# Performance work log

Hardware: AMD Instinct MI355X
Metric: run time of the kernel (lower is better)

The kernel has to match this reference:

```python
import jax, jax.numpy as jnp
import numpy as np

H = 512  # hidden_size
A = 1.0  # hard_sigm slope


def hard_sigm(a, x):
    return jnp.clip((a * x + 1.0) / 2.0, 0.0, 1.0)


def setup_inputs() -> dict:
    key = jax.random.key(0)
    ks = jax.random.split(key, 10)
    B = 8192
    bottom, top = 512, 512
    stdv = 1.0 / np.sqrt(H)
    u = lambda k, shp: jax.random.uniform(k, shp, jnp.float32, -stdv, stdv)
    return {
        "c": jax.random.normal(ks[0], (H, B), jnp.float32),
        "h_bottom": jax.random.normal(ks[1], (bottom, B), jnp.float32),
        "h": jax.random.normal(ks[2], (H, B), jnp.float32),
        "h_top": jax.random.normal(ks[3], (top, B), jnp.float32),
        "z": jax.random.uniform(ks[4], (1, B), jnp.float32),
        "z_bottom": jax.random.uniform(ks[5], (1, B), jnp.float32),
        "U_11": u(ks[6], (4 * H + 1, H)),
        "U_21": u(ks[7], (4 * H + 1, top)),
        "W_01": u(ks[8], (4 * H + 1, bottom)),
        "bias": u(ks[9], (4 * H + 1,)),
    }


def reference(c, h_bottom, h, h_top, z, z_bottom, U_11, U_21, W_01, bias):
    # z, z_bottom: (1, B) boundary indicators broadcast over the gate axis
    s_recur = (1.0 - z) * (U_11 @ h)          # (4H+1, B)
    s_topdown = z * (U_21 @ h_top)            # last_layer=False
    s_bottomup = z_bottom * (W_01 @ h_bottom)
    f_s = s_recur + s_topdown + s_bottomup + bias[:, None]

    f = jax.nn.sigmoid(f_s[0:H, :])
    i = jax.nn.sigmoid(f_s[H:2 * H, :])
    o = jax.nn.sigmoid(f_s[2 * H:3 * H, :])
    g = jnp.tanh(f_s[3 * H:4 * H, :])
    z_hat = hard_sigm(A, f_s[4 * H:4 * H + 1, :])  # (1, B)

    ig = i * g
    c_new = z * ig + (1.0 - z) * (1.0 - z_bottom) * c \
        + (1.0 - z) * z_bottom * (f * c + ig)
    tanh_c = jnp.tanh(c_new)
    h_new = z * o * tanh_c + (1.0 - z) * (1.0 - z_bottom) * h \
        + (1.0 - z) * z_bottom * o * tanh_c
    return (h_new, c_new, z_hat)
```

## Files before the change

kernel.cpp:

```cpp
#include <hip/hip_runtime.h>
#include <hip/hip_bf16.h>

#define HH 512
#define BB 8192
#define KK 1536
#define NT 48
#define HB 4194304
#define BLOB 8192

typedef __bf16 bhalf;
typedef __bf16 bf16x8 __attribute__((ext_vector_type(8)));
typedef float  f32x4  __attribute__((ext_vector_type(4)));

typedef __attribute__((address_space(1))) void* as1_t;
typedef __attribute__((address_space(3))) void* as3_t;

#define GLDS(src, dst) __builtin_amdgcn_global_load_lds((as1_t)(void*)(src), (as3_t)(void*)(dst), 16, 0, 0)
#define SBAR() asm volatile("s_barrier" ::: "memory")
#define VM0()  asm volatile("s_waitcnt vmcnt(0)" ::: "memory")


__global__ __launch_bounds__(256) void prep_all(
    const float* __restrict__ h, const float* __restrict__ ht,
    const float* __restrict__ hb, const float* __restrict__ z,
    const float* __restrict__ zb, const float* __restrict__ U11,
    const float* __restrict__ U21, const float* __restrict__ W01,
    bhalf* __restrict__ XtP, bhalf* __restrict__ WcP,
    float* __restrict__ zpart)
{
    const int tid = threadIdx.x;
    const int b   = blockIdx.x;

    if (b < 1536) {
        __shared__ float tile[32][257];
        const int kt = b % 48;
        const int nt = b / 48;
        const int n  = nt * 256 + tid;
        const int kb = kt * 32;

        const float* src; const float* wsrc; int kr; float scale;
        if (kb < 512)       { src = h;  wsrc = U11 + (size_t)2048 * 512 + kb;
                              kr = kb;        scale = 1.f - z[n]; }
        else if (kb < 1024) { src = ht; wsrc = U21 + (size_t)2048 * 512 + (kb - 512);
                              kr = kb - 512;  scale = z[n]; }
        else                { src = hb; wsrc = W01 + (size_t)2048 * 512 + (kb - 1024);
                              kr = kb - 1024; scale = zb[n]; }

        float zp = 0.f;
        #pragma unroll
        for (int kk = 0; kk < 32; ++kk) {
            const float v = src[(size_t)(kr + kk) * BB + n] * scale;
            tile[kk][tid] = v;
            zp += v * wsrc[kk];
        }
        zpart[(size_t)kt * BB + n] = zp;
        __syncthreads();

        bhalf* blob = XtP + (size_t)(nt * NT + kt) * BLOB;
        #pragma unroll
        for (int q = 0; q < 4; ++q) {
            const int s  = q * 256 + tid;
            const int rb = s >> 6, w = s & 63;
            const int hh = w >> 4, lrr = w & 15;
            const int nloc = rb * 16 + lrr, kloc = hh * 8;
            bf16x8 r;
            #pragma unroll
            for (int e = 0; e < 8; ++e) r[e] = (bhalf)tile[kloc + e][nloc];
            *(bf16x8*)(blob + s * 8) = r;
        }
    } else {
        const int o    = (b - 1536) * 4 + (tid >> 6);
        const int lane = tid & 63;
        const int g = o >> 9, j = o & 511;
        const int mp = 4 * j + g;
        const int mt = mp >> 8, rb = (mp >> 4) & 15, lrr = mp & 15;

        #pragma unroll
        for (int p = 0; p < 3; ++p) {
            const float* src = (p == 0) ? U11 : (p == 1) ? U21 : W01;
            const float* rp  = src + (size_t)o * 512 + lane * 8;
            float4 v0 = *(const float4*)rp;
            float4 v1 = *(const float4*)(rp + 4);
            bf16x8 r;
            r[0]=(bhalf)v0.x; r[1]=(bhalf)v0.y; r[2]=(bhalf)v0.z; r[3]=(bhalf)v0.w;
            r[4]=(bhalf)v1.x; r[5]=(bhalf)v1.y; r[6]=(bhalf)v1.z; r[7]=(bhalf)v1.w;
            const int kt = p * 16 + (lane >> 2);
            const int hh = lane & 3;
            *(bf16x8*)(WcP + (size_t)(mt * NT + kt) * BLOB
                       + rb * 512 + hh * 128 + lrr * 8) = r;
        }
    }
}

__device__ __forceinline__ float sigmf(float x)    { return 1.f / (1.f + __expf(-x)); }
__device__ __forceinline__ float tanhfast(float x) { return 2.f / (1.f + __expf(-2.f * x)) - 1.f; }

__global__ __launch_bounds__(512, 4) void gemm_fused(
    const bhalf* __restrict__ WcP, const bhalf* __restrict__ XtP,
    const float* __restrict__ bias, const float* __restrict__ c_in,
    const float* __restrict__ h_in, const float* __restrict__ z,
    const float* __restrict__ zb, const float* __restrict__ zpart,
    float* __restrict__ out)
{
    __shared__ bhalf As[2][BLOB];
    __shared__ bhalf Bs[2][BLOB / 2];

    const int tid  = threadIdx.x;
    const int lane = tid & 63;
    const int wid  = tid >> 6;
    const int wm   = wid >> 1, wn = wid & 1;
    const int lr   = lane & 15, hi = lane >> 4;
    const int soff = hi * 128 + lr * 8;

    const int xcd = blockIdx.x & 7;
    const int i   = blockIdx.x >> 3;
    const int mt  = ((xcd & 3) << 1) | (i & 1);
    const int nt2 = ((xcd >> 2) << 5) | (i >> 1);
    const int n0 = nt2 * 128;
    const int jb = mt * 64;

    const bhalf* gA = WcP + (size_t)mt * (NT * BLOB) + tid * 8;
    const bhalf* gB = XtP + (size_t)(nt2 >> 1) * (NT * BLOB)
                          + (nt2 & 1) * (BLOB / 2) + tid * 8;

    const bhalf* pA0 = &As[0][wm * 2048 + soff];
    const bhalf* pA1 = &As[1][wm * 2048 + soff];
    const bhalf* pB0 = &Bs[0][wn * 2048 + soff];
    const bhalf* pB1 = &Bs[1][wn * 2048 + soff];

#define STAGE(t, bf) do {                                                     \
        const bhalf* sa_ = gA + (size_t)(t) * BLOB;                           \
        const bhalf* sb_ = gB + (size_t)(t) * BLOB;                           \
        GLDS(sa_,        &As[bf][tid * 8]);                                   \
        GLDS(sa_ + 4096, &As[bf][tid * 8 + 4096]);                            \
        GLDS(sb_,        &Bs[bf][tid * 8]);                                   \
    } while (0)

#define MF(mi, ni, A_, B_) acc[mi][ni] = \
    __builtin_amdgcn_mfma_f32_16x16x32_bf16(A_, B_, acc[mi][ni], 0, 0, 0)

#define CT(q) do {                                                            \
    bf16x8 b0 = *(const bf16x8*)(pB##q);                                      \
    bf16x8 b1 = *(const bf16x8*)(pB##q + 512);                                \
    bf16x8 b2 = *(const bf16x8*)(pB##q + 1024);                               \
    bf16x8 b3 = *(const bf16x8*)(pB##q + 1536);                               \
    bf16x8 a0 = *(const bf16x8*)(pA##q);                                      \
    bf16x8 a1 = *(const bf16x8*)(pA##q + 512);                                \
    bf16x8 a2 = *(const bf16x8*)(pA##q + 1024);                               \
    bf16x8 a3 = *(const bf16x8*)(pA##q + 1536);                               \
    __builtin_amdgcn_s_setprio(1);                                            \
    MF(0,0,a0,b0); MF(0,1,a0,b1); MF(0,2,a0,b2); MF(0,3,a0,b3);               \
    MF(1,0,a1,b0); MF(1,1,a1,b1); MF(1,2,a1,b2); MF(1,3,a1,b3);               \
    MF(2,0,a2,b0); MF(2,1,a2,b1); MF(2,2,a2,b2); MF(2,3,a2,b3);               \
    MF(3,0,a3,b0); MF(3,1,a3,b1); MF(3,2,a3,b2); MF(3,3,a3,b3);               \
    __builtin_amdgcn_s_setprio(0);                                            \
} while (0)

    f32x4 acc[4][4] = {};

    STAGE(0, 0);

    if (mt == 0 && tid < 128) {
        const int n = n0 + tid;
        float s = 0.f;
        #pragma unroll
        for (int kt2 = 0; kt2 < NT; ++kt2) s += zpart[(size_t)kt2 * BB + n];
        const float v = (s + bias[2048] + 1.f) * 0.5f;
        out[(size_t)2 * HB + n] = fminf(fmaxf(v, 0.f), 1.f);
    }

    for (int t = 0; t < 46; t += 2) {
        VM0(); SBAR(); STAGE(t + 1, 1); CT(0);
        VM0(); SBAR(); STAGE(t + 2, 0); CT(1);
    }
    VM0(); SBAR(); STAGE(47, 1); CT(0);
    VM0(); SBAR(); CT(1);

    const int colbase = n0 + wn * 64 + lr;
    const int jloc0   = wm * 16 + hi;
    float zc[4], zbc[4];
    #pragma unroll
    for (int ni = 0; ni < 4; ++ni) {
        zc[ni]  = z[colbase + ni * 16];
        zbc[ni] = zb[colbase + ni * 16];
    }
    #pragma unroll
    for (int mi = 0; mi < 4; ++mi) {
        const int j = jb + jloc0 + mi * 4;
        const float bf_ = bias[j];
        const float bi_ = bias[512 + j];
        const float bo_ = bias[1024 + j];
        const float bg_ = bias[1536 + j];
        #pragma unroll
        for (int ni = 0; ni < 4; ++ni) {
            const int col = colbase + ni * 16;
            const size_t idx = (size_t)j * BB + col;
            const float cv = c_in[idx];
            const float hv = h_in[idx];
            const float fv = sigmf(acc[mi][ni][0] + bf_);
            const float iv = sigmf(acc[mi][ni][1] + bi_);
            const float ov = sigmf(acc[mi][ni][2] + bo_);
            const float gv = tanhfast(acc[mi][ni][3] + bg_);
            const float ig = iv * gv;
            const float zq = zc[ni], zbq = zbc[ni];
            const float cn = zq * ig + (1.f - zq) * (1.f - zbq) * cv
                           + (1.f - zq) * zbq * (fv * cv + ig);
            const float tc = tanhfast(cn);
            const float hn = (zq + (1.f - zq) * zbq) * ov * tc
                           + (1.f - zq) * (1.f - zbq) * hv;
            out[idx]      = hn;
            out[HB + idx] = cn;
        }
    }
}

extern "C" void kernel_launch(void* const* d_in, const int* in_sizes, int n_in,
                              void* d_out, int out_size, void* d_ws, size_t ws_size,
                              hipStream_t stream) {
    const float* c    = (const float*)d_in[0];
    const float* hb   = (const float*)d_in[1];
    const float* h    = (const float*)d_in[2];
    const float* ht   = (const float*)d_in[3];
    const float* z    = (const float*)d_in[4];
    const float* zb   = (const float*)d_in[5];
    const float* U11  = (const float*)d_in[6];
    const float* U21  = (const float*)d_in[7];
    const float* W01  = (const float*)d_in[8];
    const float* bias = (const float*)d_in[9];
    float* out = (float*)d_out;

    char* ws = (char*)d_ws;
    bhalf* XtP   = (bhalf*)ws;
    bhalf* WcP   = (bhalf*)(ws + 25165824);
    float* zpart = (float*)(ws + 25165824 + 6291456);

    prep_all  <<<2048, 256, 0, stream>>>(h, ht, hb, z, zb, U11, U21, W01,
                                         XtP, WcP, zpart);
    gemm_fused<<<512, 512, 0, stream>>>(WcP, XtP, bias, c, h, z, zb,
                                        zpart, out);
}
```

Baseline: 74.44 us.

## Enlarge GEMM tile to 256x256 with two-slab K stages and split waitcnts

Output tiles of the fused gate GEMM grow from 64 gate rows by 128 columns to 256 by 256. Each block now runs 8 waves in a 2x4 arrangement with a 32x64 tile per wave, and the grid shrinks to 256 blocks. Each pipeline stage loads two K-slabs into double-buffered LDS, with partial vmcnt waits and finer barrier-separated MFMA chunks so loads overlap compute. The aim is more operand reuse and less global/LDS traffic per MFMA. In exchange it uses more LDS and registers (launch bounds occupancy 4 to 2), leaves fewer blocks than CUs, and adds many barriers.

Measured after the change: 80.72 us. +8.4%, slower.

```diff
diff --git a/kernel.cpp b/kernel.cpp
--- a/kernel.cpp
+++ b/kernel.cpp
@@ -5,6 +5,7 @@
 #define BB 8192
 #define KK 1536
 #define NT 48
+#define NT2 24
 #define HB 4194304
 #define BLOB 8192
 
@@ -17,6 +18,8 @@
 
 #define GLDS(src, dst) __builtin_amdgcn_global_load_lds((as1_t)(void*)(src), (as3_t)(void*)(dst), 16, 0, 0)
 #define SBAR() asm volatile("s_barrier" ::: "memory")
+#define VM8()  asm volatile("s_waitcnt vmcnt(8)" ::: "memory")
+#define VM4()  asm volatile("s_waitcnt vmcnt(4)" ::: "memory")
 #define VM0()  asm volatile("s_waitcnt vmcnt(0)" ::: "memory")
 
 
@@ -95,89 +98,108 @@
 __device__ __forceinline__ float sigmf(float x)    { return 1.f / (1.f + __expf(-x)); }
 __device__ __forceinline__ float tanhfast(float x) { return 2.f / (1.f + __expf(-2.f * x)) - 1.f; }
 
-__global__ __launch_bounds__(512, 4) void gemm_fused(
+__global__ __launch_bounds__(512, 2) void gemm_fused(
     const bhalf* __restrict__ WcP, const bhalf* __restrict__ XtP,
     const float* __restrict__ bias, const float* __restrict__ c_in,
     const float* __restrict__ h_in, const float* __restrict__ z,
     const float* __restrict__ zb, const float* __restrict__ zpart,
     float* __restrict__ out)
 {
-    __shared__ bhalf As[2][BLOB];
-    __shared__ bhalf Bs[2][BLOB / 2];
+    __shared__ bhalf As[2][2][BLOB];
+    __shared__ bhalf Bs[2][2][BLOB];
 
     const int tid  = threadIdx.x;
     const int lane = tid & 63;
     const int wid  = tid >> 6;
-    const int wm   = wid >> 1, wn = wid & 1;
+    const int wm   = wid >> 2, wn = wid & 3;
     const int lr   = lane & 15, hi = lane >> 4;
     const int soff = hi * 128 + lr * 8;
 
     const int xcd = blockIdx.x & 7;
     const int i   = blockIdx.x >> 3;
-    const int mt  = ((xcd & 3) << 1) | (i & 1);
-    const int nt2 = ((xcd >> 2) << 5) | (i >> 1);
-    const int n0 = nt2 * 128;
-    const int jb = mt * 64;
-
-    const bhalf* gA = WcP + (size_t)mt * (NT * BLOB) + tid * 8;
-    const bhalf* gB = XtP + (size_t)(nt2 >> 1) * (NT * BLOB)
-                          + (nt2 & 1) * (BLOB / 2) + tid * 8;
-
-    const bhalf* pA0 = &As[0][wm * 2048 + soff];
-    const bhalf* pA1 = &As[1][wm * 2048 + soff];
-    const bhalf* pB0 = &Bs[0][wn * 2048 + soff];
-    const bhalf* pB1 = &Bs[1][wn * 2048 + soff];
-
-#define STAGE(t, bf) do {                                                     \
-        const bhalf* sa_ = gA + (size_t)(t) * BLOB;                           \
-        const bhalf* sb_ = gB + (size_t)(t) * BLOB;                           \
-        GLDS(sa_,        &As[bf][tid * 8]);                                   \
-        GLDS(sa_ + 4096, &As[bf][tid * 8 + 4096]);                            \
-        GLDS(sb_,        &Bs[bf][tid * 8]);                                   \
-    } while (0)
-
-#define MF(mi, ni, A_, B_) acc[mi][ni] = \
-    __builtin_amdgcn_mfma_f32_16x16x32_bf16(A_, B_, acc[mi][ni], 0, 0, 0)
-
-#define CT(q) do {                                                            \
-    bf16x8 b0 = *(const bf16x8*)(pB##q);                                      \
-    bf16x8 b1 = *(const bf16x8*)(pB##q + 512);                                \
-    bf16x8 b2 = *(const bf16x8*)(pB##q + 1024);                               \
-    bf16x8 b3 = *(const bf16x8*)(pB##q + 1536);                               \
-    bf16x8 a0 = *(const bf16x8*)(pA##q);                                      \
-    bf16x8 a1 = *(const bf16x8*)(pA##q + 512);                                \
-    bf16x8 a2 = *(const bf16x8*)(pA##q + 1024);                               \
-    bf16x8 a3 = *(const bf16x8*)(pA##q + 1536);                               \
-    __builtin_amdgcn_s_setprio(1);                                            \
-    MF(0,0,a0,b0); MF(0,1,a0,b1); MF(0,2,a0,b2); MF(0,3,a0,b3);               \
-    MF(1,0,a1,b0); MF(1,1,a1,b1); MF(1,2,a1,b2); MF(1,3,a1,b3);               \
-    MF(2,0,a2,b0); MF(2,1,a2,b1); MF(2,2,a2,b2); MF(2,3,a2,b3);               \
-    MF(3,0,a3,b0); MF(3,1,a3,b1); MF(3,2,a3,b2); MF(3,3,a3,b3);               \
-    __builtin_amdgcn_s_setprio(0);                                            \
-} while (0)
-
-    f32x4 acc[4][4] = {};
-
-    STAGE(0, 0);
-
-    if (mt == 0 && tid < 128) {
+    const int mt  = i & 7;
+    const int nt  = xcd * 4 + (i >> 3);
+    const int m0 = mt * 256, n0 = nt * 256;
+
+    if (mt == 0 && tid < 256) {
         const int n = n0 + tid;
         float s = 0.f;
         #pragma unroll
         for (int kt2 = 0; kt2 < NT; ++kt2) s += zpart[(size_t)kt2 * BB + n];
         const float v = (s + bias[2048] + 1.f) * 0.5f;
         out[(size_t)2 * HB + n] = fminf(fmaxf(v, 0.f), 1.f);
-    }
-
-    for (int t = 0; t < 46; t += 2) {
-        VM0(); SBAR(); STAGE(t + 1, 1); CT(0);
-        VM0(); SBAR(); STAGE(t + 2, 0); CT(1);
-    }
-    VM0(); SBAR(); STAGE(47, 1); CT(0);
-    VM0(); SBAR(); CT(1);
+        VM0();
+    }
+
+    const bhalf* gA = WcP + (size_t)mt * (NT * BLOB) + tid * 8;
+    const bhalf* gB = XtP + (size_t)nt * (NT * BLOB) + tid * 8;
+
+    const bhalf* pa00 = &As[0][0][wm * 4096 + soff];
+    const bhalf* pa01 = &As[0][1][wm * 4096 + soff];
+    const bhalf* pa10 = &As[1][0][wm * 4096 + soff];
+    const bhalf* pa11 = &As[1][1][wm * 4096 + soff];
+    const bhalf* pb00 = &Bs[0][0][wn * 2048 + soff];
+    const bhalf* pb01 = &Bs[0][1][wn * 2048 + soff];
+    const bhalf* pb10 = &Bs[1][0][wn * 2048 + soff];
+    const bhalf* pb11 = &Bs[1][1][wn * 2048 + soff];
+
+#define STG(t2, kh, nb) do {                                                  \
+        const bhalf* sa_ = gA + (size_t)((t2) * 2 + (kh)) * BLOB;             \
+        const bhalf* sb_ = gB + (size_t)((t2) * 2 + (kh)) * BLOB;             \
+        GLDS(sa_,        &As[nb][kh][tid * 8]);                               \
+        GLDS(sa_ + 4096, &As[nb][kh][tid * 8 + 4096]);                        \
+        GLDS(sb_,        &Bs[nb][kh][tid * 8]);                               \
+        GLDS(sb_ + 4096, &Bs[nb][kh][tid * 8 + 4096]);                        \
+    } while (0)
+
+#define MF(mi, ni, A_, B_) acc[mi][ni] = \
+    __builtin_amdgcn_mfma_f32_16x16x32_bf16(A_, B_, acc[mi][ni], 0, 0, 0)
+
+#define CL(mb) do { __builtin_amdgcn_s_setprio(1);                            \
+    MF(mb+0,0,a0,b0); MF(mb+0,1,a0,b1); MF(mb+0,2,a0,b2); MF(mb+0,3,a0,b3);   \
+    MF(mb+1,0,a1,b0); MF(mb+1,1,a1,b1); MF(mb+1,2,a1,b2); MF(mb+1,3,a1,b3);   \
+    MF(mb+2,0,a2,b0); MF(mb+2,1,a2,b1); MF(mb+2,2,a2,b2); MF(mb+2,3,a2,b3);   \
+    MF(mb+3,0,a3,b0); MF(mb+3,1,a3,b1); MF(mb+3,2,a3,b2); MF(mb+3,3,a3,b3);   \
+    __builtin_amdgcn_s_setprio(0); } while (0)
+
+#define RDA4(P, off) do {                                                     \
+    a0 = *(const bf16x8*)(P + (off));        a1 = *(const bf16x8*)(P + (off) + 512);  \
+    a2 = *(const bf16x8*)(P + (off) + 1024); a3 = *(const bf16x8*)(P + (off) + 1536); } while (0)
+#define RDB4(P) do {                                                          \
+    b0 = *(const bf16x8*)(P);        b1 = *(const bf16x8*)(P + 512);          \
+    b2 = *(const bf16x8*)(P + 1024); b3 = *(const bf16x8*)(P + 1536); } while (0)
+
+#define TILE(AB0, AB1, BB0, BB1, NB_, TS, DOST, VMP1, VMP3) do {              \
+                                                             \
+    RDB4(BB0); RDA4(AB0, 0);                                                  \
+    if (DOST) STG(TS, 0, NB_);                                                \
+    SBAR(); CL(0); SBAR();                                                    \
+                                               \
+    RDA4(AB0, 2048);                                                          \
+    if (DOST) STG(TS, 1, NB_);                                                \
+    VMP1; SBAR(); CL(4); SBAR();                                              \
+                                                             \
+    RDB4(BB1); RDA4(AB1, 0);                                                  \
+    SBAR(); CL(0); SBAR();                                                    \
+                                                             \
+    RDA4(AB1, 2048);                                                          \
+    VMP3; SBAR(); CL(4); SBAR();                                              \
+} while (0)
+
+    f32x4 acc[8][4] = {};
+    bf16x8 a0, a1, a2, a3, b0, b1, b2, b3;
+
+    STG(0, 0, 0); STG(0, 1, 0);
+    VM4(); SBAR();
+
+    for (int t = 0; t < 22; t += 2) {
+        TILE(pa00, pa01, pb00, pb01, 1, t + 1, 1, VM8(), VM4());
+        TILE(pa10, pa11, pb10, pb11, 0, t + 2, 1, VM8(), VM4());
+    }
+    TILE(pa00, pa01, pb00, pb01, 1, 23, 1, VM8(), VM4());
+    TILE(pa10, pa11, pb10, pb11, 0, 0, 0, VM0(), ((void)0));
 
     const int colbase = n0 + wn * 64 + lr;
-    const int jloc0   = wm * 16 + hi;
     float zc[4], zbc[4];
     #pragma unroll
     for (int ni = 0; ni < 4; ++ni) {
@@ -185,8 +207,8 @@
         zbc[ni] = zb[colbase + ni * 16];
     }
     #pragma unroll
-    for (int mi = 0; mi < 4; ++mi) {
-        const int j = jb + jloc0 + mi * 4;
+    for (int mi = 0; mi < 8; ++mi) {
+        const int j = (m0 >> 2) + wm * 32 + mi * 4 + hi;
         const float bf_ = bias[j];
         const float bi_ = bias[512 + j];
         const float bo_ = bias[1024 + j];
@@ -236,6 +258,6 @@
 
     prep_all  <<<2048, 256, 0, stream>>>(h, ht, hb, z, zb, U11, U21, W01,
                                          XtP, WcP, zpart);
-    gemm_fused<<<512, 512, 0, stream>>>(WcP, XtP, bias, c, h, z, zb,
+    gemm_fused<<<256, 512, 0, stream>>>(WcP, XtP, bias, c, h, z, zb,
                                         zpart, out);
 }
```
